# Performance work log

Hardware: AMD Instinct MI355X
Metric: run time of the kernel (lower is better)

The kernel has to match this reference:

```python
import jax, jax.numpy as jnp
import numpy as np

EPS = 1e-8

def q2r(q):
    # q: [N,4] (w,x,y,z), normalized before use. Returns [N,3,3] rotation matrices.
    q = q / jnp.linalg.norm(q, axis=-1, keepdims=True)
    w, x, y, z = q[:, 0], q[:, 1], q[:, 2], q[:, 3]
    R = jnp.stack([
        1 - 2 * (y * y + z * z), 2 * (x * y - w * z),     2 * (x * z + w * y),
        2 * (x * y + w * z),     1 - 2 * (x * x + z * z), 2 * (y * z - w * x),
        2 * (x * z - w * y),     2 * (y * z + w * x),     1 - 2 * (x * x + y * y),
    ], axis=-1)
    return R.reshape(-1, 3, 3)

def setup_inputs() -> dict:
    key = jax.random.key(0)
    k1, k2 = jax.random.split(key)
    N = 4_000_000
    quaternion = jax.random.normal(k1, (N, 4), dtype=jnp.float32)
    scale = jax.random.normal(k2, (N, 3), dtype=jnp.float32)
    return {"quaternion": quaternion, "scale": scale}

def reference(quaternion, scale):
    # get_gaussian_3d_cov with scale_activation='abs'
    R = q2r(quaternion)                      # [N,3,3]
    s = jnp.abs(scale) + EPS                 # [N,3]
    RS = R * s[:, None, :]                   # R @ diag(s), fused (no diag_embed)
    RSSR = jnp.einsum('nij,nkj->nik', RS, RS)  # RS @ RS^T -> [N,3,3]
    return RSSR
```

## Files before the change

kernel.cpp:

```cpp
#include <hip/hip_runtime.h>

#define EPS 1e-8f
#define BLOCK 256
#define GPT 2
#define TILE (BLOCK * GPT)

typedef float fvec4 __attribute__((ext_vector_type(4)));

__global__ __launch_bounds__(BLOCK) void gaussians_cov_kernel(
    const fvec4* __restrict__ quat,
    const float* __restrict__ scale,
    fvec4*       __restrict__ out4,
    int n)
{
    __shared__ float s_out[TILE * 9];

    const int t    = threadIdx.x;
    const int base = blockIdx.x * TILE;

    #pragma unroll
    for (int g = 0; g < GPT; ++g) {
        const int lt = t + g * BLOCK;
        const int i  = base + lt;
        if (i < n) {
            fvec4 q = __builtin_nontemporal_load(&quat[i]);
            float w = q.x, x = q.y, y = q.z, z = q.w;

            float n2 = w*w + x*x + y*y + z*z;
            float t2 = 2.0f / n2;

            float xx = x*x*t2, yy = y*y*t2, zz = z*z*t2;
            float xy = x*y*t2, xz = x*z*t2, yz = y*z*t2;
            float wx = w*x*t2, wy = w*y*t2, wz = w*z*t2;

            float r00 = 1.0f - yy - zz, r01 = xy - wz,        r02 = xz + wy;
            float r10 = xy + wz,        r11 = 1.0f - xx - zz, r12 = yz - wx;
            float r20 = xz - wy,        r21 = yz + wx,        r22 = 1.0f - xx - yy;

            float s0 = fabsf(__builtin_nontemporal_load(&scale[3*i + 0])) + EPS;
            float s1 = fabsf(__builtin_nontemporal_load(&scale[3*i + 1])) + EPS;
            float s2 = fabsf(__builtin_nontemporal_load(&scale[3*i + 2])) + EPS;
            float a = s0*s0, b = s1*s1, c = s2*s2;

            float m00 = r00*r00*a + r01*r01*b + r02*r02*c;
            float m01 = r00*r10*a + r01*r11*b + r02*r12*c;
            float m02 = r00*r20*a + r01*r21*b + r02*r22*c;
            float m11 = r10*r10*a + r11*r11*b + r12*r12*c;
            float m12 = r10*r20*a + r11*r21*b + r12*r22*c;
            float m22 = r20*r20*a + r21*r21*b + r22*r22*c;

            float* o = s_out + 9*lt;
            o[0] = m00; o[1] = m01; o[2] = m02;
            o[3] = m01; o[4] = m11; o[5] = m12;
            o[6] = m02; o[7] = m12; o[8] = m22;
        }
    }
    __syncthreads();

    {
        const int obase4 = blockIdx.x * (TILE * 9 / 4);
        const long long otot4 = (9LL * n) / 4;
        #pragma unroll
        for (int j = t; j < TILE * 9 / 4; j += BLOCK) {
            long long go = obase4 + (long long)j;
            if (go < otot4)
                __builtin_nontemporal_store(((fvec4*)s_out)[j], &out4[go]);
        }
    }
}

extern "C" void kernel_launch(void* const* d_in, const int* in_sizes, int n_in,
                              void* d_out, int out_size, void* d_ws, size_t ws_size,
                              hipStream_t stream) {
    const fvec4* quat  = (const fvec4*)d_in[0];
    const float* scale = (const float*)d_in[1];
    fvec4* out4 = (fvec4*)d_out;
    int n = in_sizes[0] / 4;

    int grid = (n + TILE - 1) / TILE;
    gaussians_cov_kernel<<<grid, BLOCK, 0, stream>>>(quat, scale, out4, n);
}
```

Baseline: 218.1 us.

## Stage scale through LDS with vec4 coalesced loads and prefetch quaternions

Scale values are now loaded cooperatively as 16-byte vectors into shared memory instead of three strided scalar loads per thread. Quaternion loads are hoisted ahead of the barrier so all global reads are issued together. Block size doubles to 512, which doubles the per-block tile and raises shared memory use. The goal is more coalesced, better-overlapped input traffic, at the cost of an extra barrier and lower occupancy per CU. A tail with 3n not divisible by 4 would leave the last scale values unloaded.

```diff
diff --git a/kernel.cpp b/kernel.cpp
--- a/kernel.cpp
+++ b/kernel.cpp
@@ -1,7 +1,7 @@
 #include <hip/hip_runtime.h>
 
 #define EPS 1e-8f
-#define BLOCK 256
+#define BLOCK 512
 #define GPT 2
 #define TILE (BLOCK * GPT)
 
@@ -9,22 +9,42 @@
 
 __global__ __launch_bounds__(BLOCK) void gaussians_cov_kernel(
     const fvec4* __restrict__ quat,
-    const float* __restrict__ scale,
+    const fvec4* __restrict__ scale4,
     fvec4*       __restrict__ out4,
     int n)
 {
+    __shared__ float s_scale[TILE * 3];
     __shared__ float s_out[TILE * 9];
 
     const int t    = threadIdx.x;
     const int base = blockIdx.x * TILE;
+
+    {
+        const int sbase4 = blockIdx.x * (TILE * 3 / 4);
+        const int stot4  = (3 * n) / 4;
+        #pragma unroll
+        for (int j = t; j < TILE * 3 / 4; j += BLOCK) {
+            int gi = sbase4 + j;
+            if (gi < stot4)
+                ((fvec4*)s_scale)[j] = __builtin_nontemporal_load(&scale4[gi]);
+        }
+    }
+
+    fvec4 q[GPT];
+    #pragma unroll
+    for (int g = 0; g < GPT; ++g) {
+        int i = base + t + g * BLOCK;
+        if (i < n) q[g] = __builtin_nontemporal_load(&quat[i]);
+    }
+
+    __syncthreads();
 
     #pragma unroll
     for (int g = 0; g < GPT; ++g) {
         const int lt = t + g * BLOCK;
         const int i  = base + lt;
         if (i < n) {
-            fvec4 q = __builtin_nontemporal_load(&quat[i]);
-            float w = q.x, x = q.y, y = q.z, z = q.w;
+            float w = q[g].x, x = q[g].y, y = q[g].z, z = q[g].w;
 
             float n2 = w*w + x*x + y*y + z*z;
             float t2 = 2.0f / n2;
@@ -37,9 +57,9 @@
             float r10 = xy + wz,        r11 = 1.0f - xx - zz, r12 = yz - wx;
             float r20 = xz - wy,        r21 = yz + wx,        r22 = 1.0f - xx - yy;
 
-            float s0 = fabsf(__builtin_nontemporal_load(&scale[3*i + 0])) + EPS;
-            float s1 = fabsf(__builtin_nontemporal_load(&scale[3*i + 1])) + EPS;
-            float s2 = fabsf(__builtin_nontemporal_load(&scale[3*i + 2])) + EPS;
+            float s0 = fabsf(s_scale[3*lt + 0]) + EPS;
+            float s1 = fabsf(s_scale[3*lt + 1]) + EPS;
+            float s2 = fabsf(s_scale[3*lt + 2]) + EPS;
             float a = s0*s0, b = s1*s1, c = s2*s2;
 
             float m00 = r00*r00*a + r01*r01*b + r02*r02*c;
@@ -58,8 +78,8 @@
     __syncthreads();
 
     {
-        const int obase4 = blockIdx.x * (TILE * 9 / 4);
-        const long long otot4 = (9LL * n) / 4;
+        const long long obase4 = (long long)blockIdx.x * (TILE * 9 / 4);
+        const long long otot4  = (9LL * n) / 4;
         #pragma unroll
         for (int j = t; j < TILE * 9 / 4; j += BLOCK) {
             long long go = obase4 + (long long)j;
@@ -72,11 +92,11 @@
 extern "C" void kernel_launch(void* const* d_in, const int* in_sizes, int n_in,
                               void* d_out, int out_size, void* d_ws, size_t ws_size,
                               hipStream_t stream) {
-    const fvec4* quat  = (const fvec4*)d_in[0];
-    const float* scale = (const float*)d_in[1];
+    const fvec4* quat   = (const fvec4*)d_in[0];
+    const fvec4* scale4 = (const fvec4*)d_in[1];
     fvec4* out4 = (fvec4*)d_out;
     int n = in_sizes[0] / 4;
 
     int grid = (n + TILE - 1) / TILE;
-    gaussians_cov_kernel<<<grid, BLOCK, 0, stream>>>(quat, scale, out4, n);
+    gaussians_cov_kernel<<<grid, BLOCK, 0, stream>>>(quat, scale4, out4, n);
 }
```

Result: no change. 217.5 us (-0.3%).
